# Kernel tuning notes

Hardware: AMD Instinct MI355X
Metric: run time of the kernel (lower is better)

The kernel has to match this reference:

```python
import jax, jax.numpy as jnp
import numpy as np

N_ENV, N_STEP = 4096, 2048
GAMMA, LAMBDA = 0.99, 0.95


def setup_inputs() -> dict:
    key = jax.random.key(0)
    k1, k2, k3 = jax.random.split(key, 3)
    rewards = jax.random.normal(k1, (N_ENV, N_STEP), dtype=jnp.float32)
    values = jax.random.normal(k2, (N_ENV, N_STEP + 1), dtype=jnp.float32)
    first = (jax.random.uniform(k3, (N_ENV, N_STEP + 1)) < 0.01).astype(jnp.float32)
    return {"rewards": rewards, "values": values, "first": first}


def reference(rewards, values, first):
    """GAE backward recurrence, vectorized over envs via a reverse lax.scan.

    advantages[t] = delta[t] + notlast[t]*gamma*lambda*advantages[t+1]
    delta[t]      = r[t] + notlast[t]*gamma*V[t+1] - V[t]
    """
    notlast = 1.0 - first[:, 1:]                        # [E, T]
    delta = rewards + notlast * GAMMA * values[:, 1:] - values[:, :-1]  # [E, T]

    def step(lastgaelam, xs):
        d_t, nl_t = xs                                  # each [E]
        adv_t = d_t + nl_t * (GAMMA * LAMBDA) * lastgaelam
        return adv_t, adv_t

    init = jnp.zeros(rewards.shape[0], dtype=rewards.dtype)
    _, advs = jax.lax.scan(step, init, (delta.T, notlast.T), reverse=True)
    advantages = advs.T                                 # [E, T]
    v_targ = values[:, :-1] + advantages
    return advantages, v_targ
```

## Files before the change

kernel.cpp:

```cpp
#include <hip/hip_runtime.h>


constexpr int NE   = 4096;
constexpr int NT   = 2048;
constexpr int NT1  = 2049;
constexpr float GAMMA  = 0.99f;
constexpr float LAMBDA = 0.95f;
constexpr int TPB = 256;
constexpr int PER = NT / TPB;

__global__ __launch_bounds__(TPB) void gae_kernel(
    const float* __restrict__ rewards,
    const float* __restrict__ values,
    const float* __restrict__ first,
    float* __restrict__ out)
{
    const int e   = blockIdx.x;
    const int tid = threadIdx.x;
    const int t0  = tid * PER;

    const float* r_row = rewards + (size_t)e * NT;
    const float* v_row = values  + (size_t)e * NT1;
    const float* f_row = first   + (size_t)e * NT1;

    float r[PER];
    {
        const float4 ra = *reinterpret_cast<const float4*>(r_row + t0);
        const float4 rb = *reinterpret_cast<const float4*>(r_row + t0 + 4);
        r[0]=ra.x; r[1]=ra.y; r[2]=ra.z; r[3]=ra.w;
        r[4]=rb.x; r[5]=rb.y; r[6]=rb.z; r[7]=rb.w;
    }

    float v[PER + 1];
#pragma unroll
    for (int k = 0; k <= PER; ++k) v[k] = v_row[t0 + k];

    float c[PER], d[PER];
#pragma unroll
    for (int k = 0; k < PER; ++k) {
        const float nl = 1.0f - f_row[t0 + 1 + k];
        d[k] = r[k] + nl * GAMMA * v[k + 1] - v[k];
        c[k] = nl * (GAMMA * LAMBDA);
    }

    float A = 1.0f, B = 0.0f;
#pragma unroll
    for (int k = PER - 1; k >= 0; --k) {
        B = d[k] + c[k] * B;
        A *= c[k];
    }

    __shared__ float sA[TPB];
    __shared__ float sB[TPB];
    float cA = A, cB = B;
#pragma unroll
    for (int off = 1; off < TPB; off <<= 1) {
        sA[tid] = cA;
        sB[tid] = cB;
        __syncthreads();
        if (tid + off < TPB) {
            const float a2 = sA[tid + off];
            const float b2 = sB[tid + off];
            cB = cA * b2 + cB;
            cA = cA * a2;
        }
        __syncthreads();
    }

    sB[tid] = cB;
    __syncthreads();
    const float adv_in = (tid + 1 < TPB) ? sB[tid + 1] : 0.0f;

    float adv[PER];
    float x = adv_in;
#pragma unroll
    for (int k = PER - 1; k >= 0; --k) {
        x = d[k] + c[k] * x;
        adv[k] = x;
    }

    float* adv_out = out + (size_t)e * NT + t0;
    float* vt_out  = out + (size_t)NE * NT + (size_t)e * NT + t0;
    *reinterpret_cast<float4*>(adv_out)     = make_float4(adv[0], adv[1], adv[2], adv[3]);
    *reinterpret_cast<float4*>(adv_out + 4) = make_float4(adv[4], adv[5], adv[6], adv[7]);
    *reinterpret_cast<float4*>(vt_out)      = make_float4(v[0]+adv[0], v[1]+adv[1], v[2]+adv[2], v[3]+adv[3]);
    *reinterpret_cast<float4*>(vt_out + 4)  = make_float4(v[4]+adv[4], v[5]+adv[5], v[6]+adv[6], v[7]+adv[7]);
}

extern "C" void kernel_launch(void* const* d_in, const int* in_sizes, int n_in,
                              void* d_out, int out_size, void* d_ws, size_t ws_size,
                              hipStream_t stream) {
    const float* rewards = (const float*)d_in[0];
    const float* values  = (const float*)d_in[1];
    const float* first   = (const float*)d_in[2];
    float* out = (float*)d_out;
    gae_kernel<<<NE, TPB, 0, stream>>>(rewards, values, first, out);
}
```

Baseline: 31.72 us.

## Stage GAE inputs and outputs through padded LDS for coalesced global access

Loads of rewards, values and first now use a thread-interleaved (j*TPB+tid) pattern, so each wavefront touches consecutive addresses. Each thread computes delta and the discount coefficient and writes them to padded shared-memory arrays. Threads then read back their contiguous 8-element chunk for the blocked scan. Results go back through LDS so the advantage and value-target stores are also coalesced. This aims to remove strided and unaligned per-thread global access, especially on the odd-pitched values and first rows, at the cost of about 17KB more LDS per block and two extra barriers.

```diff
diff --git a/kernel.cpp b/kernel.cpp
--- a/kernel.cpp
+++ b/kernel.cpp
@@ -9,38 +9,48 @@
 constexpr int TPB = 256;
 constexpr int PER = NT / TPB;
 
+__device__ __forceinline__ int pad(int i) { return i + (i >> 5); }
+constexpr int LDSN = NT + (NT >> 5);
+
 __global__ __launch_bounds__(TPB) void gae_kernel(
     const float* __restrict__ rewards,
     const float* __restrict__ values,
     const float* __restrict__ first,
     float* __restrict__ out)
 {
+    __shared__ float d_lds[LDSN];
+    __shared__ float c_lds[LDSN];
+    __shared__ float sA[TPB];
+    __shared__ float sB[TPB];
+
     const int e   = blockIdx.x;
     const int tid = threadIdx.x;
-    const int t0  = tid * PER;
 
     const float* r_row = rewards + (size_t)e * NT;
     const float* v_row = values  + (size_t)e * NT1;
     const float* f_row = first   + (size_t)e * NT1;
 
-    float r[PER];
-    {
-        const float4 ra = *reinterpret_cast<const float4*>(r_row + t0);
-        const float4 rb = *reinterpret_cast<const float4*>(r_row + t0 + 4);
-        r[0]=ra.x; r[1]=ra.y; r[2]=ra.z; r[3]=ra.w;
-        r[4]=rb.x; r[5]=rb.y; r[6]=rb.z; r[7]=rb.w;
+    float vreg[PER];
+#pragma unroll
+    for (int j = 0; j < PER; ++j) {
+        const int t = j * TPB + tid;
+        const float v0 = v_row[t];
+        const float v1 = v_row[t + 1];
+        const float f1 = f_row[t + 1];
+        const float rr = r_row[t];
+        vreg[j] = v0;
+        const float nl = 1.0f - f1;
+        d_lds[pad(t)] = rr + nl * GAMMA * v1 - v0;
+        c_lds[pad(t)] = nl * (GAMMA * LAMBDA);
     }
+    __syncthreads();
 
-    float v[PER + 1];
-#pragma unroll
-    for (int k = 0; k <= PER; ++k) v[k] = v_row[t0 + k];
-
-    float c[PER], d[PER];
+    const int t0 = tid * PER;
+    float d[PER], c[PER];
 #pragma unroll
     for (int k = 0; k < PER; ++k) {
-        const float nl = 1.0f - f_row[t0 + 1 + k];
-        d[k] = r[k] + nl * GAMMA * v[k + 1] - v[k];
-        c[k] = nl * (GAMMA * LAMBDA);
+        d[k] = d_lds[pad(t0 + k)];
+        c[k] = c_lds[pad(t0 + k)];
     }
 
     float A = 1.0f, B = 0.0f;
@@ -50,8 +60,6 @@
         A *= c[k];
     }
 
-    __shared__ float sA[TPB];
-    __shared__ float sB[TPB];
     float cA = A, cB = B;
 #pragma unroll
     for (int off = 1; off < TPB; off <<= 1) {
@@ -66,25 +74,29 @@
         }
         __syncthreads();
     }
-
     sB[tid] = cB;
     __syncthreads();
     const float adv_in = (tid + 1 < TPB) ? sB[tid + 1] : 0.0f;
 
-    float adv[PER];
     float x = adv_in;
 #pragma unroll
     for (int k = PER - 1; k >= 0; --k) {
         x = d[k] + c[k] * x;
-        adv[k] = x;
+        d[k] = x;
     }
+#pragma unroll
+    for (int k = 0; k < PER; ++k) d_lds[pad(t0 + k)] = d[k];
+    __syncthreads();
 
-    float* adv_out = out + (size_t)e * NT + t0;
-    float* vt_out  = out + (size_t)NE * NT + (size_t)e * NT + t0;
-    *reinterpret_cast<float4*>(adv_out)     = make_float4(adv[0], adv[1], adv[2], adv[3]);
-    *reinterpret_cast<float4*>(adv_out + 4) = make_float4(adv[4], adv[5], adv[6], adv[7]);
-    *reinterpret_cast<float4*>(vt_out)      = make_float4(v[0]+adv[0], v[1]+adv[1], v[2]+adv[2], v[3]+adv[3]);
-    *reinterpret_cast<float4*>(vt_out + 4)  = make_float4(v[4]+adv[4], v[5]+adv[5], v[6]+adv[6], v[7]+adv[7]);
+    float* __restrict__ adv_out = out + (size_t)e * NT;
+    float* __restrict__ vt_out  = out + (size_t)NE * NT + (size_t)e * NT;
+#pragma unroll
+    for (int j = 0; j < PER; ++j) {
+        const int t = j * TPB + tid;
+        const float a = d_lds[pad(t)];
+        adv_out[t] = a;
+        vt_out[t]  = vreg[j] + a;
+    }
 }
 
 extern "C" void kernel_launch(void* const* d_in, const int* in_sizes, int n_in,
```

New measurement: 30.42 us. 4.1% less time.

## Coalesce global loads/stores via swizzled LDS staging and use wave-shuffle scan

Applied to the files above, without the earlier changes.

Global reads and writes are restructured so consecutive threads touch consecutive float4 chunks, with d/c coefficients and results staged through XOR-swizzled shared memory to hand each thread its contiguous 8-step segment. The block-wide Hillis-Steele scan over LDS with many barriers is replaced by an intra-wavefront shuffle scan plus a small cross-wave combine of four wave totals. Output stores become nontemporal. This targets uncoalesced strided access and barrier overhead, at the cost of extra LDS traffic and more registers.

```diff
diff --git a/kernel.cpp b/kernel.cpp
--- a/kernel.cpp
+++ b/kernel.cpp
@@ -8,6 +8,12 @@
 constexpr float LAMBDA = 0.95f;
 constexpr int TPB = 256;
 constexpr int PER = NT / TPB;
+constexpr int NQ  = NT / 4;
+constexpr int QPT = NQ / TPB;
+
+typedef float f32x4 __attribute__((ext_vector_type(4)));
+
+__device__ __forceinline__ int swz(int g) { return g ^ ((g >> 3) & 7); }
 
 __global__ __launch_bounds__(TPB) void gae_kernel(
     const float* __restrict__ rewards,
@@ -15,76 +21,114 @@
     const float* __restrict__ first,
     float* __restrict__ out)
 {
-    const int e   = blockIdx.x;
-    const int tid = threadIdx.x;
-    const int t0  = tid * PER;
+    __shared__ float4 d_lds[NQ];
+    __shared__ float4 c_lds[NQ];
+    __shared__ float  sWA[4];
+    __shared__ float  sWB[4];
+
+    const int e    = blockIdx.x;
+    const int tid  = threadIdx.x;
+    const int lane = tid & 63;
+    const int w    = tid >> 6;
 
     const float* r_row = rewards + (size_t)e * NT;
     const float* v_row = values  + (size_t)e * NT1;
     const float* f_row = first   + (size_t)e * NT1;
 
-    float r[PER];
+    float4 vreg[QPT];
+#pragma unroll
+    for (int j = 0; j < QPT; ++j) {
+        const int q = j * TPB + tid;
+        const int t = 4 * q;
+        const float4 r4 = *reinterpret_cast<const float4*>(r_row + t);
+        const float v0 = v_row[t + 0];
+        const float v1 = v_row[t + 1];
+        const float v2 = v_row[t + 2];
+        const float v3 = v_row[t + 3];
+        const float v4 = v_row[t + 4];
+        const float n0 = 1.0f - f_row[t + 1];
+        const float n1 = 1.0f - f_row[t + 2];
+        const float n2 = 1.0f - f_row[t + 3];
+        const float n3 = 1.0f - f_row[t + 4];
+        vreg[j] = make_float4(v0, v1, v2, v3);
+        float4 d4, c4;
+        d4.x = r4.x + n0 * GAMMA * v1 - v0;  c4.x = n0 * (GAMMA * LAMBDA);
+        d4.y = r4.y + n1 * GAMMA * v2 - v1;  c4.y = n1 * (GAMMA * LAMBDA);
+        d4.z = r4.z + n2 * GAMMA * v3 - v2;  c4.z = n2 * (GAMMA * LAMBDA);
+        d4.w = r4.w + n3 * GAMMA * v4 - v3;  c4.w = n3 * (GAMMA * LAMBDA);
+        d_lds[swz(q)] = d4;
+        c_lds[swz(q)] = c4;
+    }
+    __syncthreads();
+
+    float d[PER], c[PER];
     {
-        const float4 ra = *reinterpret_cast<const float4*>(r_row + t0);
-        const float4 rb = *reinterpret_cast<const float4*>(r_row + t0 + 4);
-        r[0]=ra.x; r[1]=ra.y; r[2]=ra.z; r[3]=ra.w;
-        r[4]=rb.x; r[5]=rb.y; r[6]=rb.z; r[7]=rb.w;
-    }
-
-    float v[PER + 1];
-#pragma unroll
-    for (int k = 0; k <= PER; ++k) v[k] = v_row[t0 + k];
-
-    float c[PER], d[PER];
-#pragma unroll
-    for (int k = 0; k < PER; ++k) {
-        const float nl = 1.0f - f_row[t0 + 1 + k];
-        d[k] = r[k] + nl * GAMMA * v[k + 1] - v[k];
-        c[k] = nl * (GAMMA * LAMBDA);
+        const float4 da = d_lds[swz(2 * tid)];
+        const float4 db = d_lds[swz(2 * tid + 1)];
+        const float4 ca = c_lds[swz(2 * tid)];
+        const float4 cb = c_lds[swz(2 * tid + 1)];
+        d[0]=da.x; d[1]=da.y; d[2]=da.z; d[3]=da.w;
+        d[4]=db.x; d[5]=db.y; d[6]=db.z; d[7]=db.w;
+        c[0]=ca.x; c[1]=ca.y; c[2]=ca.z; c[3]=ca.w;
+        c[4]=cb.x; c[5]=cb.y; c[6]=cb.z; c[7]=cb.w;
     }
 
     float A = 1.0f, B = 0.0f;
 #pragma unroll
     for (int k = PER - 1; k >= 0; --k) {
-        B = d[k] + c[k] * B;
+        B = fmaf(c[k], B, d[k]);
         A *= c[k];
     }
 
-    __shared__ float sA[TPB];
-    __shared__ float sB[TPB];
     float cA = A, cB = B;
 #pragma unroll
-    for (int off = 1; off < TPB; off <<= 1) {
-        sA[tid] = cA;
-        sB[tid] = cB;
-        __syncthreads();
-        if (tid + off < TPB) {
-            const float a2 = sA[tid + off];
-            const float b2 = sB[tid + off];
-            cB = cA * b2 + cB;
+    for (int off = 1; off < 64; off <<= 1) {
+        const float a2 = __shfl_down(cA, off);
+        const float b2 = __shfl_down(cB, off);
+        if (lane + off < 64) {
+            cB = fmaf(cA, b2, cB);
             cA = cA * a2;
         }
-        __syncthreads();
     }
 
-    sB[tid] = cB;
+    if (lane == 0) { sWA[w] = cA; sWB[w] = cB; }
+
+    float EA = __shfl_down(cA, 1);
+    float EB = __shfl_down(cB, 1);
+    if (lane == 63) { EA = 1.0f; EB = 0.0f; }
+
     __syncthreads();
-    const float adv_in = (tid + 1 < TPB) ? sB[tid + 1] : 0.0f;
+
+    float TB = 0.0f;
+    for (int u = 3; u > w; --u) {
+        TB = fmaf(sWA[u], TB, sWB[u]);
+    }
+    float x = fmaf(EA, TB, EB);
 
     float adv[PER];
-    float x = adv_in;
 #pragma unroll
     for (int k = PER - 1; k >= 0; --k) {
-        x = d[k] + c[k] * x;
+        x = fmaf(c[k], x, d[k]);
         adv[k] = x;
     }
+    d_lds[swz(2 * tid)]     = make_float4(adv[0], adv[1], adv[2], adv[3]);
+    d_lds[swz(2 * tid + 1)] = make_float4(adv[4], adv[5], adv[6], adv[7]);
+    __syncthreads();
 
-    float* adv_out = out + (size_t)e * NT + t0;
-    float* vt_out  = out + (size_t)NE * NT + (size_t)e * NT + t0;
-    *reinterpret_cast<float4*>(adv_out)     = make_float4(adv[0], adv[1], adv[2], adv[3]);
-    *reinterpret_cast<float4*>(adv_out + 4) = make_float4(adv[4], adv[5], adv[6], adv[7]);
-    *reinterpret_cast<float4*>(vt_out)      = make_float4(v[0]+adv[0], v[1]+adv[1], v[2]+adv[2], v[3]+adv[3]);
-    *reinterpret_cast<float4*>(vt_out + 4)  = make_float4(v[4]+adv[4], v[5]+adv[5], v[6]+adv[6], v[7]+adv[7]);
+    float* __restrict__ adv_out = out + (size_t)e * NT;
+    float* __restrict__ vt_out  = out + (size_t)NE * NT + (size_t)e * NT;
+#pragma unroll
+    for (int j = 0; j < QPT; ++j) {
+        const int q = j * TPB + tid;
+        const int t = 4 * q;
+        const float4 a4 = d_lds[swz(q)];
+        const float4 v4 = vreg[j];
+        f32x4 av; av.x = a4.x; av.y = a4.y; av.z = a4.z; av.w = a4.w;
+        f32x4 vt; vt.x = v4.x + a4.x; vt.y = v4.y + a4.y;
+                  vt.z = v4.z + a4.z; vt.w = v4.w + a4.w;
+        __builtin_nontemporal_store(av, reinterpret_cast<f32x4*>(adv_out + t));
+        __builtin_nontemporal_store(vt, reinterpret_cast<f32x4*>(vt_out + t));
+    }
 }
 
 extern "C" void kernel_launch(void* const* d_in, const int* in_sizes, int n_in,
```

New measurement: 30.05 us. 5.3% less time.
